# Kernel optimization log

Measured on AMD Instinct MI355X. Metric: run time of the kernel, lower is better.

Reference implementation:

```python
import jax, jax.numpy as jnp
import numpy as np

N = 100000
E = 1600000
D_IN = 128
HEADS = 4
C = 16  # hidden // heads
NEG_SLOPE = 0.2


def setup_inputs() -> dict:
    key = jax.random.key(0)
    ks = jax.random.split(key, 8)
    x = jax.random.normal(ks[0], (N, D_IN), dtype=jnp.float32)
    edge_index = jax.random.randint(ks[1], (2, E), 0, N, dtype=jnp.int32)
    s = 1.0 / np.sqrt(D_IN)
    W_l = jax.random.normal(ks[2], (D_IN, HEADS * C), dtype=jnp.float32) * s
    b_l = jnp.zeros((HEADS * C,), dtype=jnp.float32)
    W_r = jax.random.normal(ks[3], (D_IN, HEADS * C), dtype=jnp.float32) * s
    b_r = jnp.zeros((HEADS * C,), dtype=jnp.float32)
    att = jax.random.normal(ks[4], (HEADS, C), dtype=jnp.float32) * (1.0 / np.sqrt(C))
    bias = jnp.zeros((HEADS * C,), dtype=jnp.float32)
    W_head = jax.random.normal(ks[5], (HEADS * C, 1), dtype=jnp.float32) * (1.0 / np.sqrt(HEADS * C))
    b_head = jnp.zeros((1,), dtype=jnp.float32)
    return {"x": x, "edge_index": edge_index, "W_l": W_l, "b_l": b_l,
            "W_r": W_r, "b_r": b_r, "att": att, "bias": bias,
            "W_head": W_head, "b_head": b_head}


def reference(x, edge_index, W_l, b_l, W_r, b_r, att, bias, W_head, b_head):
    # GATv2Conv (PyG semantics, add_self_loops=True, concat=True)
    n = x.shape[0]
    # add self loops
    loops = jnp.arange(n, dtype=edge_index.dtype)
    src = jnp.concatenate([edge_index[0], loops])  # source j
    dst = jnp.concatenate([edge_index[1], loops])  # target i
    # per-node linear projections -> [N, H, C]
    x_l = (x @ W_l + b_l).reshape(n, HEADS, C)
    x_r = (x @ W_r + b_r).reshape(n, HEADS, C)
    # per-edge attention logits: att . LeakyReLU(x_l[j] + x_r[i])
    e = x_l[src] + x_r[dst]                               # [E', H, C]
    e = jnp.where(e >= 0, e, NEG_SLOPE * e)
    logits = jnp.einsum('ehc,hc->eh', e, att)             # [E', H]
    # segment softmax over incoming edges of each target node
    seg_max = jax.ops.segment_max(logits, dst, num_segments=n)  # [N, H]
    expw = jnp.exp(logits - seg_max[dst])
    seg_sum = jax.ops.segment_sum(expw, dst, num_segments=n)
    alpha = expw / seg_sum[dst]                           # [E', H]
    # weighted scatter-aggregate of source messages
    msg = alpha[:, :, None] * x_l[src]                    # [E', H, C]
    out = jax.ops.segment_sum(msg, dst, num_segments=n)   # [N, H, C]
    out = out.reshape(n, HEADS * C) + bias
    # ReLU + Linear head
    h = jax.nn.relu(out)
    return (h @ W_head + b_head).squeeze(-1)              # [N]
```

## Files before the change

kernel.cpp:

```cpp
#include <hip/hip_runtime.h>
#include <hip/hip_bf16.h>
#include <hip/hip_fp16.h>

#define HC 64
#define D_IN 128
#define NEG_SLOPE 0.2f
#define BCAP 8192
#define L2E 1.44269504f

using f32x4 = __attribute__((ext_vector_type(4))) float;
using f16x8 = __attribute__((ext_vector_type(8))) _Float16;
using f16x2 = __attribute__((ext_vector_type(2))) _Float16;

__global__ void k_iota(int* __restrict__ p, int n) {
    int i = blockIdx.x * blockDim.x + threadIdx.x;
    if (i < n) p[i] = i * BCAP;
}

__global__ __launch_bounds__(256, 3) void k_proj(
    const float* __restrict__ x,
    const float* __restrict__ Wl, const float* __restrict__ bl,
    const float* __restrict__ Wr, const float* __restrict__ br,
    __half* __restrict__ xlh, float* __restrict__ xr, int N) {
    __shared__ _Float16 sWT[128 * 136];
    __shared__ _Float16 sX[32 * 136];
    const int t = threadIdx.x;
    for (int idx = t; idx < 8192; idx += 256) {
        const int k = idx >> 6;
        const int c = idx & 63;
        sWT[c * 136 + k]        = (_Float16)Wl[idx];
        sWT[(c + 64) * 136 + k] = (_Float16)Wr[idx];
    }
    const int lane = t & 63;
    const int wave = t >> 6;
    const int m = lane & 15;
    const int q = lane >> 4;
    float bfu[2];
#pragma unroll
    for (int cc = 0; cc < 2; ++cc) {
        const int ct = wave * 2 + cc;
        const int ch = (ct & 3) * 16 + m;
        bfu[cc] = (ct < 4) ? bl[ch] : br[ch];
    }
    __syncthreads();

    const int ntrip = N >> 5;
    for (int trip = blockIdx.x; trip < ntrip; trip += gridDim.x) {
        const int i0 = trip << 5;
        for (int c = t; c < 1024; c += 256) {
            const int r = c >> 5, c4 = c & 31;
            float4 v = ((const float4*)(x + (size_t)(i0 + r) * D_IN))[c4];
            _Float16* dp = &sX[r * 136 + c4 * 4];
            dp[0] = (_Float16)v.x; dp[1] = (_Float16)v.y;
            dp[2] = (_Float16)v.z; dp[3] = (_Float16)v.w;
        }
        __syncthreads();
        f16x8 af[2][4];
#pragma unroll
        for (int tt = 0; tt < 2; ++tt)
#pragma unroll
            for (int kk = 0; kk < 4; ++kk)
                af[tt][kk] = *(const f16x8*)&sX[(tt * 16 + m) * 136 + kk * 32 + q * 8];
#pragma unroll
        for (int cc = 0; cc < 2; ++cc) {
            const int ct = wave * 2 + cc;
            const _Float16* bp = &sWT[(ct * 16 + m) * 136 + q * 8];
            f32x4 acc0 = {0.f, 0.f, 0.f, 0.f};
            f32x4 acc1 = {0.f, 0.f, 0.f, 0.f};
#pragma unroll
            for (int kk = 0; kk < 4; ++kk) {
                f16x8 bf = *(const f16x8*)(bp + kk * 32);
                acc0 = __builtin_amdgcn_mfma_f32_16x16x32_f16(af[0][kk], bf, acc0, 0, 0, 0);
                acc1 = __builtin_amdgcn_mfma_f32_16x16x32_f16(af[1][kk], bf, acc1, 0, 0, 0);
            }
            const float bv = bfu[cc];
            if (ct < 4) {
                const int ch = ct * 16 + m;
#pragma unroll
                for (int r = 0; r < 4; ++r) {
                    xlh[(size_t)(i0 + q * 4 + r) * HC + ch]      = __float2half(acc0[r] + bv);
                    xlh[(size_t)(i0 + 16 + q * 4 + r) * HC + ch] = __float2half(acc1[r] + bv);
                }
            } else {
                const int ch = (ct - 4) * 16 + m;
#pragma unroll
                for (int r = 0; r < 4; ++r) {
                    xr[(size_t)(i0 + q * 4 + r) * HC + ch]      = acc0[r] + bv;
                    xr[(size_t)(i0 + 16 + q * 4 + r) * HC + ch] = acc1[r] + bv;
                }
            }
        }
        __syncthreads();
    }
}

__global__ __launch_bounds__(256) void k_scat1(const int* __restrict__ src,
                                               const int* __restrict__ dst, int E,
                                               int* __restrict__ bfill,
                                               unsigned* __restrict__ coarse) {
    __shared__ int h[512], bl[512], cur[512];
    for (int t = threadIdx.x; t < 512; t += 256) { h[t] = 0; cur[t] = 0; }
    __syncthreads();
    const int beg = blockIdx.x * 4096;
    const int end = min(beg + 4096, E);
    for (int p = beg + threadIdx.x; p < end; p += 256)
        atomicAdd(&h[dst[p] >> 8], 1);
    __syncthreads();
    for (int t = threadIdx.x; t < 512; t += 256)
        bl[t] = h[t] ? atomicAdd(&bfill[t], h[t]) : 0;
    __syncthreads();
    for (int p = beg + threadIdx.x; p < end; p += 256) {
        const int d = dst[p];
        const int bin = d >> 8;
        const int r = atomicAdd(&cur[bin], 1);
        coarse[bl[bin] + r] = ((unsigned)src[p] << 8) | (unsigned)(d & 255);
    }
}

__global__ __launch_bounds__(256) void k_sort2(const unsigned* __restrict__ coarse,
                                               const int* __restrict__ bfill,
                                               int* __restrict__ row_off,
                                               int* __restrict__ endo,
                                               int* __restrict__ sorted_src, int N) {
    __shared__ int cnt[256], lds[256];
    const int t = threadIdx.x;
    const int b = blockIdx.x;
    const int eb = b * BCAP;
    const int ee = bfill[b];
    cnt[t] = 0;
    __syncthreads();
    for (int p = eb + t; p < ee; p += 256)
        atomicAdd(&cnt[coarse[p] & 255], 1);
    __syncthreads();
    const int c = cnt[t];
    lds[t] = c;
    __syncthreads();
    for (int o = 1; o < 256; o <<= 1) {
        int v = (t >= o) ? lds[t - o] : 0;
        __syncthreads();
        lds[t] += v;
        __syncthreads();
    }
    const int ex = lds[t] - c;
    const int node = (b << 8) + t;
    if (node < N) {
        row_off[node] = eb + ex;
        endo[node]    = eb + ex + c;
    }
    __syncthreads();
    cnt[t] = ex;
    __syncthreads();
    for (int p = eb + t; p < ee; p += 256) {
        const unsigned e = coarse[p];
        const int r = atomicAdd(&cnt[e & 255], 1);
        sorted_src[eb + r] = (int)(e >> 8);
    }
}

__device__ __forceinline__ float redpair(float v) {
    int a = __builtin_amdgcn_update_dpp(0, __float_as_int(v), 0xB1, 0xF, 0xF, true);
    return v + __int_as_float(a);
}

__global__ __launch_bounds__(256) void k_agg(
    const __half* __restrict__ xlh, const float* __restrict__ xr,
    const float* __restrict__ att, const float* __restrict__ bias,
    const float* __restrict__ Wh, const float* __restrict__ bh,
    const int* __restrict__ row_off, const int* __restrict__ endo,
    const int* __restrict__ sorted_src, float* __restrict__ out, int N) {
    const int wave = threadIdx.x >> 6;
    const int lane = threadIdx.x & 63;
    const int i = blockIdx.x * 4 + wave;
    if (i >= N) return;
    const int sub  = lane & 7;
    const int slot = lane >> 3;

    const _Float16* xlhp = (const _Float16*)xlh;
    const float4 atA = *(const float4*)(att + 8 * sub);
    const float4 atB = *(const float4*)(att + 8 * sub + 4);
    f16x2 at[4];
    at[0][0] = (_Float16)(atA.x * L2E); at[0][1] = (_Float16)(atA.y * L2E);
    at[1][0] = (_Float16)(atA.z * L2E); at[1][1] = (_Float16)(atA.w * L2E);
    at[2][0] = (_Float16)(atB.x * L2E); at[2][1] = (_Float16)(atB.y * L2E);
    at[3][0] = (_Float16)(atB.z * L2E); at[3][1] = (_Float16)(atB.w * L2E);
    const f16x2 c02 = {(_Float16)NEG_SLOPE, (_Float16)NEG_SLOPE};

    const float4 xrA = *(const float4*)(xr + ((size_t)i << 6) + 8 * sub);
    const float4 xrB = *(const float4*)(xr + ((size_t)i << 6) + 8 * sub + 4);
    f16x2 xri[4];
    xri[0][0] = (_Float16)xrA.x; xri[0][1] = (_Float16)xrA.y;
    xri[1][0] = (_Float16)xrA.z; xri[1][1] = (_Float16)xrA.w;
    xri[2][0] = (_Float16)xrB.x; xri[2][1] = (_Float16)xrB.y;
    xri[3][0] = (_Float16)xrB.z; xri[3][1] = (_Float16)xrB.w;

    const uint4 xliraw = *(const uint4*)(xlhp + ((size_t)i << 6) + 8 * sub);
    f16x2 xli[4];
    xli[0] = __builtin_bit_cast(f16x2, xliraw.x);
    xli[1] = __builtin_bit_cast(f16x2, xliraw.y);
    xli[2] = __builtin_bit_cast(f16x2, xliraw.z);
    xli[3] = __builtin_bit_cast(f16x2, xliraw.w);

    float t0 = 0.f;
#pragma unroll
    for (int c = 0; c < 4; ++c) {
        f16x2 w = xli[c] + xri[c];
        w = __builtin_elementwise_max(w, w * c02);
        t0 = __builtin_amdgcn_fdot2(at[c], w, t0, false);
    }
    t0 = redpair(t0);
    const float pe0 = (slot == 0) ? exp2f(t0) : 0.f;
    float s = pe0;
    float a[8];
#pragma unroll
    for (int c = 0; c < 4; ++c) {
        a[2 * c]     = pe0 * (float)xli[c][0];
        a[2 * c + 1] = pe0 * (float)xli[c][1];
    }

    int p = row_off[i];
    const int end = endo[i];

#define EDGE_GROUP(JEXPR, PRED)                                              \
    {                                                                        \
        const int jj = (JEXPR);                                              \
        const uint4 raw = *(const uint4*)(xlhp + ((size_t)jj << 6) + 8 * sub);\
        f16x2 xv[4];                                                         \
        xv[0] = __builtin_bit_cast(f16x2, raw.x);                            \
        xv[1] = __builtin_bit_cast(f16x2, raw.y);                            \
        xv[2] = __builtin_bit_cast(f16x2, raw.z);                            \
        xv[3] = __builtin_bit_cast(f16x2, raw.w);                            \
        float tt = 0.f;                                                      \
        _Pragma("unroll")                                                    \
        for (int c = 0; c < 4; ++c) {                                        \
            f16x2 w = xv[c] + xri[c];                                        \
            w = __builtin_elementwise_max(w, w * c02);                       \
            tt = __builtin_amdgcn_fdot2(at[c], w, tt, false);                \
        }                                                                    \
        tt = redpair(tt);                                                    \
        const float pe = (PRED) ? exp2f(tt) : 0.f;                           \
        s += pe;                                                             \
        _Pragma("unroll")                                                    \
        for (int c = 0; c < 4; ++c) {                                        \
            a[2 * c]     = fmaf(pe, (float)xv[c][0], a[2 * c]);              \
            a[2 * c + 1] = fmaf(pe, (float)xv[c][1], a[2 * c + 1]);          \
        }                                                                    \
    }

    for (; p + 16 <= end; p += 16) {
        const int j0 = sorted_src[p + slot];
        const int j1 = sorted_src[p + 8 + slot];
        EDGE_GROUP(j0, true)
        EDGE_GROUP(j1, true)
    }
    if (p + 8 <= end) {
        const int j0 = sorted_src[p + slot];
        EDGE_GROUP(j0, true)
        p += 8;
    }
    const int rem = end - p;
    if (rem > 0) {
        const int idx = p + slot;
        const int j0 = sorted_src[(idx < end) ? idx : (end - 1)];
        EDGE_GROUP(j0, slot < rem)
    }
#undef EDGE_GROUP

    s += __shfl_xor(s, 8);  s += __shfl_xor(s, 16);  s += __shfl_xor(s, 32);
#pragma unroll
    for (int c = 0; c < 8; ++c) {
        a[c] += __shfl_xor(a[c], 8);
        a[c] += __shfl_xor(a[c], 16);
        a[c] += __shfl_xor(a[c], 32);
    }

    const float4 biA = *(const float4*)(bias + 8 * sub);
    const float4 biB = *(const float4*)(bias + 8 * sub + 4);
    const float4 whA = *(const float4*)(Wh + 8 * sub);
    const float4 whB = *(const float4*)(Wh + 8 * sub + 4);
    const float inv = 1.f / s;
    float y = fmaxf(a[0] * inv + biA.x, 0.f) * whA.x
            + fmaxf(a[1] * inv + biA.y, 0.f) * whA.y
            + fmaxf(a[2] * inv + biA.z, 0.f) * whA.z
            + fmaxf(a[3] * inv + biA.w, 0.f) * whA.w
            + fmaxf(a[4] * inv + biB.x, 0.f) * whB.x
            + fmaxf(a[5] * inv + biB.y, 0.f) * whB.y
            + fmaxf(a[6] * inv + biB.z, 0.f) * whB.z
            + fmaxf(a[7] * inv + biB.w, 0.f) * whB.w;
    y += __shfl_xor(y, 1);
    y += __shfl_xor(y, 2);
    y += __shfl_xor(y, 4);
    if (lane == 0) out[i] = y + bh[0];
}

extern "C" void kernel_launch(void* const* d_in, const int* in_sizes, int n_in,
                              void* d_out, int out_size, void* d_ws, size_t ws_size,
                              hipStream_t stream) {
    const float* x   = (const float*)d_in[0];
    const int*   ei  = (const int*)d_in[1];
    const float* Wl  = (const float*)d_in[2];
    const float* bl  = (const float*)d_in[3];
    const float* Wr  = (const float*)d_in[4];
    const float* br  = (const float*)d_in[5];
    const float* att = (const float*)d_in[6];
    const float* bias= (const float*)d_in[7];
    const float* Wh  = (const float*)d_in[8];
    const float* bh  = (const float*)d_in[9];
    float* out = (float*)d_out;

    const int N = in_sizes[0] / D_IN;
    const int E = in_sizes[1] / 2;
    const int* src = ei;
    const int* dst = ei + E;
    const int nbkt = (N + 255) / 256;

    auto align = [](size_t v) { return (v + 255) & ~(size_t)255; };
    char* ws = (char*)d_ws;
    size_t off = 0;
    __half* xlh     = (__half*)(ws + off);   off = align(off + (size_t)N * HC * 2);
    float* xr       = (float*)(ws + off);    off = align(off + (size_t)N * HC * 4);
    int*   row_off  = (int*)(ws + off);      off = align(off + (size_t)N * 4);
    int*   endo     = (int*)(ws + off);      off = align(off + (size_t)N * 4);
    int*   bfill    = (int*)(ws + off);      off = align(off + 512 * 4);
    int*   sorted   = (int*)(ws + off);      off = align(off + (size_t)nbkt * BCAP * 4);
    unsigned* coarse= (unsigned*)(ws + off); off = align(off + (size_t)nbkt * BCAP * 4);
    (void)ws_size;

    k_iota<<<2, 256, 0, stream>>>(bfill, 512);

    k_proj<<<1024, 256, 0, stream>>>(x, Wl, bl, Wr, br, xlh, xr, N);

    k_scat1<<<(E + 4095) / 4096, 256, 0, stream>>>(src, dst, E, bfill, coarse);
    k_sort2<<<nbkt, 256, 0, stream>>>(coarse, bfill, row_off, endo, sorted, N);

    k_agg<<<(N + 3) / 4, 256, 0, stream>>>(xlh, xr, att, bias, Wh, bh,
                                           row_off, endo, sorted, out, N);
}
```

Before: 226.1 us.

## Fuse per-bucket CSR sort into aggregation kernel with 64-node LDS buckets

Drops the separate second-pass sort kernel. Edges are now bucketed into 64-node bins, and each aggregation block sorts its bin's edges by destination in shared memory before its four waves process 16 nodes each. This removes the global writes and reads of sorted_src, row_off and endo, plus one launch. The scatter pass now reads edges with vectorized int4 loads. In exchange there are far fewer blocks, each wave works through its nodes one after another, bucket capacity is fixed at 1536 edges, and the dynamically indexed edge register array may spill.

```diff
diff --git a/kernel.cpp b/kernel.cpp
--- a/kernel.cpp
+++ b/kernel.cpp
@@ -5,7 +5,9 @@
 #define HC 64
 #define D_IN 128
 #define NEG_SLOPE 0.2f
-#define BCAP 8192
+#define BK 64
+#define BCAP2 1536
+#define NBIN 2048
 #define L2E 1.44269504f
 
 using f32x4 = __attribute__((ext_vector_type(4))) float;
@@ -14,7 +16,7 @@
 
 __global__ void k_iota(int* __restrict__ p, int n) {
     int i = blockIdx.x * blockDim.x + threadIdx.x;
-    if (i < n) p[i] = i * BCAP;
+    if (i < n) p[i] = i * BCAP2;
 }
 
 __global__ __launch_bounds__(256, 3) void k_proj(
@@ -98,62 +100,45 @@
                                                const int* __restrict__ dst, int E,
                                                int* __restrict__ bfill,
                                                unsigned* __restrict__ coarse) {
-    __shared__ int h[512], bl[512], cur[512];
-    for (int t = threadIdx.x; t < 512; t += 256) { h[t] = 0; cur[t] = 0; }
+    __shared__ int h[NBIN], bl[NBIN], cur[NBIN];
+    const int t = threadIdx.x;
+    for (int i = t; i < NBIN; i += 256) { h[i] = 0; cur[i] = 0; }
     __syncthreads();
     const int beg = blockIdx.x * 4096;
-    const int end = min(beg + 4096, E);
-    for (int p = beg + threadIdx.x; p < end; p += 256)
-        atomicAdd(&h[dst[p] >> 8], 1);
-    __syncthreads();
-    for (int t = threadIdx.x; t < 512; t += 256)
-        bl[t] = h[t] ? atomicAdd(&bfill[t], h[t]) : 0;
-    __syncthreads();
-    for (int p = beg + threadIdx.x; p < end; p += 256) {
-        const int d = dst[p];
-        const int bin = d >> 8;
-        const int r = atomicAdd(&cur[bin], 1);
-        coarse[bl[bin] + r] = ((unsigned)src[p] << 8) | (unsigned)(d & 255);
-    }
-}
-
-__global__ __launch_bounds__(256) void k_sort2(const unsigned* __restrict__ coarse,
-                                               const int* __restrict__ bfill,
-                                               int* __restrict__ row_off,
-                                               int* __restrict__ endo,
-                                               int* __restrict__ sorted_src, int N) {
-    __shared__ int cnt[256], lds[256];
-    const int t = threadIdx.x;
-    const int b = blockIdx.x;
-    const int eb = b * BCAP;
-    const int ee = bfill[b];
-    cnt[t] = 0;
-    __syncthreads();
-    for (int p = eb + t; p < ee; p += 256)
-        atomicAdd(&cnt[coarse[p] & 255], 1);
-    __syncthreads();
-    const int c = cnt[t];
-    lds[t] = c;
-    __syncthreads();
-    for (int o = 1; o < 256; o <<= 1) {
-        int v = (t >= o) ? lds[t - o] : 0;
-        __syncthreads();
-        lds[t] += v;
-        __syncthreads();
-    }
-    const int ex = lds[t] - c;
-    const int node = (b << 8) + t;
-    if (node < N) {
-        row_off[node] = eb + ex;
-        endo[node]    = eb + ex + c;
-    }
-    __syncthreads();
-    cnt[t] = ex;
-    __syncthreads();
-    for (int p = eb + t; p < ee; p += 256) {
-        const unsigned e = coarse[p];
-        const int r = atomicAdd(&cnt[e & 255], 1);
-        sorted_src[eb + r] = (int)(e >> 8);
+    int4 d4[4], s4[4];
+#pragma unroll
+    for (int r = 0; r < 4; ++r) {
+        const int idx = beg + 4 * t + r * 1024;
+        if (idx < E) {
+            d4[r] = *(const int4*)(dst + idx);
+            s4[r] = *(const int4*)(src + idx);
+        } else { d4[r] = make_int4(-1, -1, -1, -1); }
+    }
+#pragma unroll
+    for (int r = 0; r < 4; ++r) {
+        if (d4[r].x >= 0) {
+            atomicAdd(&h[d4[r].x >> 6], 1);
+            atomicAdd(&h[d4[r].y >> 6], 1);
+            atomicAdd(&h[d4[r].z >> 6], 1);
+            atomicAdd(&h[d4[r].w >> 6], 1);
+        }
+    }
+    __syncthreads();
+    for (int i = t; i < NBIN; i += 256)
+        bl[i] = h[i] ? atomicAdd(&bfill[i], h[i]) : 0;
+    __syncthreads();
+#pragma unroll
+    for (int r = 0; r < 4; ++r) {
+        if (d4[r].x >= 0) {
+            const int dd[4] = {d4[r].x, d4[r].y, d4[r].z, d4[r].w};
+            const int ss[4] = {s4[r].x, s4[r].y, s4[r].z, s4[r].w};
+#pragma unroll
+            for (int j = 0; j < 4; ++j) {
+                const int bin = dd[j] >> 6;
+                const int pos = atomicAdd(&cur[bin], 1);
+                coarse[bl[bin] + pos] = ((unsigned)ss[j] << 6) | (unsigned)(dd[j] & 63);
+            }
+        }
     }
 }
 
@@ -162,20 +147,51 @@
     return v + __int_as_float(a);
 }
 
-__global__ __launch_bounds__(256) void k_agg(
+__global__ __launch_bounds__(256) void k_aggs(
     const __half* __restrict__ xlh, const float* __restrict__ xr,
     const float* __restrict__ att, const float* __restrict__ bias,
     const float* __restrict__ Wh, const float* __restrict__ bh,
-    const int* __restrict__ row_off, const int* __restrict__ endo,
-    const int* __restrict__ sorted_src, float* __restrict__ out, int N) {
-    const int wave = threadIdx.x >> 6;
-    const int lane = threadIdx.x & 63;
-    const int i = blockIdx.x * 4 + wave;
-    if (i >= N) return;
+    const int* __restrict__ bfill, const unsigned* __restrict__ coarse,
+    float* __restrict__ out, int N) {
+    __shared__ int s_src[BCAP2];
+    __shared__ int s_cnt[BK], s_off[BK], s_cur[BK], s_scan[BK];
+    const int t = threadIdx.x;
+    const int b = blockIdx.x;
+    const int eb = b * BCAP2;
+    const int ee = bfill[b];
+    if (t < BK) { s_cnt[t] = 0; s_cur[t] = 0; }
+    __syncthreads();
+    unsigned er[6]; int nr = 0;
+#pragma unroll
+    for (int r = 0; r < 6; ++r) {
+        const int idx = eb + t + r * 256;
+        if (idx < ee) er[nr++] = coarse[idx];
+    }
+    for (int k = 0; k < nr; ++k) atomicAdd(&s_cnt[er[k] & 63], 1);
+    __syncthreads();
+    if (t < BK) s_scan[t] = s_cnt[t];
+    __syncthreads();
+    for (int o = 1; o < BK; o <<= 1) {
+        int v = (t < BK && t >= o) ? s_scan[t - o] : 0;
+        __syncthreads();
+        if (t < BK) s_scan[t] += v;
+        __syncthreads();
+    }
+    if (t < BK) s_off[t] = s_scan[t] - s_cnt[t];
+    __syncthreads();
+    for (int k = 0; k < nr; ++k) {
+        const int bin = er[k] & 63;
+        const int pos = atomicAdd(&s_cur[bin], 1);
+        s_src[s_off[bin] + pos] = (int)(er[k] >> 6);
+    }
+    __syncthreads();
+
+    const int wave = t >> 6;
+    const int lane = t & 63;
     const int sub  = lane & 7;
     const int slot = lane >> 3;
-
     const _Float16* xlhp = (const _Float16*)xlh;
+
     const float4 atA = *(const float4*)(att + 8 * sub);
     const float4 atB = *(const float4*)(att + 8 * sub + 4);
     f16x2 at[4];
@@ -184,42 +200,51 @@
     at[2][0] = (_Float16)(atB.x * L2E); at[2][1] = (_Float16)(atB.y * L2E);
     at[3][0] = (_Float16)(atB.z * L2E); at[3][1] = (_Float16)(atB.w * L2E);
     const f16x2 c02 = {(_Float16)NEG_SLOPE, (_Float16)NEG_SLOPE};
-
-    const float4 xrA = *(const float4*)(xr + ((size_t)i << 6) + 8 * sub);
-    const float4 xrB = *(const float4*)(xr + ((size_t)i << 6) + 8 * sub + 4);
-    f16x2 xri[4];
-    xri[0][0] = (_Float16)xrA.x; xri[0][1] = (_Float16)xrA.y;
-    xri[1][0] = (_Float16)xrA.z; xri[1][1] = (_Float16)xrA.w;
-    xri[2][0] = (_Float16)xrB.x; xri[2][1] = (_Float16)xrB.y;
-    xri[3][0] = (_Float16)xrB.z; xri[3][1] = (_Float16)xrB.w;
-
-    const uint4 xliraw = *(const uint4*)(xlhp + ((size_t)i << 6) + 8 * sub);
-    f16x2 xli[4];
-    xli[0] = __builtin_bit_cast(f16x2, xliraw.x);
-    xli[1] = __builtin_bit_cast(f16x2, xliraw.y);
-    xli[2] = __builtin_bit_cast(f16x2, xliraw.z);
-    xli[3] = __builtin_bit_cast(f16x2, xliraw.w);
-
-    float t0 = 0.f;
-#pragma unroll
-    for (int c = 0; c < 4; ++c) {
-        f16x2 w = xli[c] + xri[c];
-        w = __builtin_elementwise_max(w, w * c02);
-        t0 = __builtin_amdgcn_fdot2(at[c], w, t0, false);
-    }
-    t0 = redpair(t0);
-    const float pe0 = (slot == 0) ? exp2f(t0) : 0.f;
-    float s = pe0;
-    float a[8];
-#pragma unroll
-    for (int c = 0; c < 4; ++c) {
-        a[2 * c]     = pe0 * (float)xli[c][0];
-        a[2 * c + 1] = pe0 * (float)xli[c][1];
-    }
-
-    int p = row_off[i];
-    const int end = endo[i];
-
+    const float4 biA = *(const float4*)(bias + 8 * sub);
+    const float4 biB = *(const float4*)(bias + 8 * sub + 4);
+    const float4 whA = *(const float4*)(Wh + 8 * sub);
+    const float4 whB = *(const float4*)(Wh + 8 * sub + 4);
+    const float bhv = bh[0];
+
+    for (int k16 = 0; k16 < 16; ++k16) {
+        const int nl = wave + 4 * k16;
+        const int i = (b << 6) + nl;
+        if (i >= N) continue;
+        const int beg = s_off[nl];
+        const int cnt = s_cnt[nl];
+
+        const float4 xrA = *(const float4*)(xr + ((size_t)i << 6) + 8 * sub);
+        const float4 xrB = *(const float4*)(xr + ((size_t)i << 6) + 8 * sub + 4);
+        f16x2 xri[4];
+        xri[0][0] = (_Float16)xrA.x; xri[0][1] = (_Float16)xrA.y;
+        xri[1][0] = (_Float16)xrA.z; xri[1][1] = (_Float16)xrA.w;
+        xri[2][0] = (_Float16)xrB.x; xri[2][1] = (_Float16)xrB.y;
+        xri[3][0] = (_Float16)xrB.z; xri[3][1] = (_Float16)xrB.w;
+        const uint4 xliraw = *(const uint4*)(xlhp + ((size_t)i << 6) + 8 * sub);
+        f16x2 xli[4];
+        xli[0] = __builtin_bit_cast(f16x2, xliraw.x);
+        xli[1] = __builtin_bit_cast(f16x2, xliraw.y);
+        xli[2] = __builtin_bit_cast(f16x2, xliraw.z);
+        xli[3] = __builtin_bit_cast(f16x2, xliraw.w);
+
+        float t0 = 0.f;
+#pragma unroll
+        for (int c = 0; c < 4; ++c) {
+            f16x2 w = xli[c] + xri[c];
+            w = __builtin_elementwise_max(w, w * c02);
+            t0 = __builtin_amdgcn_fdot2(at[c], w, t0, false);
+        }
+        t0 = redpair(t0);
+        const float pe0 = (slot == 0) ? exp2f(t0) : 0.f;
+        float s = pe0;
+        float a[8];
+#pragma unroll
+        for (int c = 0; c < 4; ++c) {
+            a[2 * c]     = pe0 * (float)xli[c][0];
+            a[2 * c + 1] = pe0 * (float)xli[c][1];
+        }
+
+        int p = 0;
 #define EDGE_GROUP(JEXPR, PRED)                                              \
     {                                                                        \
         const int jj = (JEXPR);                                              \
@@ -245,51 +270,46 @@
             a[2 * c + 1] = fmaf(pe, (float)xv[c][1], a[2 * c + 1]);          \
         }                                                                    \
     }
-
-    for (; p + 16 <= end; p += 16) {
-        const int j0 = sorted_src[p + slot];
-        const int j1 = sorted_src[p + 8 + slot];
-        EDGE_GROUP(j0, true)
-        EDGE_GROUP(j1, true)
-    }
-    if (p + 8 <= end) {
-        const int j0 = sorted_src[p + slot];
-        EDGE_GROUP(j0, true)
-        p += 8;
-    }
-    const int rem = end - p;
-    if (rem > 0) {
-        const int idx = p + slot;
-        const int j0 = sorted_src[(idx < end) ? idx : (end - 1)];
-        EDGE_GROUP(j0, slot < rem)
-    }
+        for (; p + 16 <= cnt; p += 16) {
+            const int j0 = s_src[beg + p + slot];
+            const int j1 = s_src[beg + p + 8 + slot];
+            EDGE_GROUP(j0, true)
+            EDGE_GROUP(j1, true)
+        }
+        if (p + 8 <= cnt) {
+            const int j0 = s_src[beg + p + slot];
+            EDGE_GROUP(j0, true)
+            p += 8;
+        }
+        const int rem = cnt - p;
+        if (rem > 0) {
+            const int idx = p + slot;
+            const int j0 = s_src[beg + ((idx < cnt) ? idx : (cnt - 1))];
+            EDGE_GROUP(j0, slot < rem)
+        }
 #undef EDGE_GROUP
 
-    s += __shfl_xor(s, 8);  s += __shfl_xor(s, 16);  s += __shfl_xor(s, 32);
-#pragma unroll
-    for (int c = 0; c < 8; ++c) {
-        a[c] += __shfl_xor(a[c], 8);
-        a[c] += __shfl_xor(a[c], 16);
-        a[c] += __shfl_xor(a[c], 32);
-    }
-
-    const float4 biA = *(const float4*)(bias + 8 * sub);
-    const float4 biB = *(const float4*)(bias + 8 * sub + 4);
-    const float4 whA = *(const float4*)(Wh + 8 * sub);
-    const float4 whB = *(const float4*)(Wh + 8 * sub + 4);
-    const float inv = 1.f / s;
-    float y = fmaxf(a[0] * inv + biA.x, 0.f) * whA.x
-            + fmaxf(a[1] * inv + biA.y, 0.f) * whA.y
-            + fmaxf(a[2] * inv + biA.z, 0.f) * whA.z
-            + fmaxf(a[3] * inv + biA.w, 0.f) * whA.w
-            + fmaxf(a[4] * inv + biB.x, 0.f) * whB.x
-            + fmaxf(a[5] * inv + biB.y, 0.f) * whB.y
-            + fmaxf(a[6] * inv + biB.z, 0.f) * whB.z
-            + fmaxf(a[7] * inv + biB.w, 0.f) * whB.w;
-    y += __shfl_xor(y, 1);
-    y += __shfl_xor(y, 2);
-    y += __shfl_xor(y, 4);
-    if (lane == 0) out[i] = y + bh[0];
+        s += __shfl_xor(s, 8);  s += __shfl_xor(s, 16);  s += __shfl_xor(s, 32);
+#pragma unroll
+        for (int c = 0; c < 8; ++c) {
+            a[c] += __shfl_xor(a[c], 8);
+            a[c] += __shfl_xor(a[c], 16);
+            a[c] += __shfl_xor(a[c], 32);
+        }
+        const float inv = 1.f / s;
+        float y = fmaxf(a[0] * inv + biA.x, 0.f) * whA.x
+                + fmaxf(a[1] * inv + biA.y, 0.f) * whA.y
+                + fmaxf(a[2] * inv + biA.z, 0.f) * whA.z
+                + fmaxf(a[3] * inv + biA.w, 0.f) * whA.w
+                + fmaxf(a[4] * inv + biB.x, 0.f) * whB.x
+                + fmaxf(a[5] * inv + biB.y, 0.f) * whB.y
+                + fmaxf(a[6] * inv + biB.z, 0.f) * whB.z
+                + fmaxf(a[7] * inv + biB.w, 0.f) * whB.w;
+        y += __shfl_xor(y, 1);
+        y += __shfl_xor(y, 2);
+        y += __shfl_xor(y, 4);
+        if (lane == 0) out[i] = y + bhv;
+    }
 }
 
 extern "C" void kernel_launch(void* const* d_in, const int* in_sizes, int n_in,
@@ -311,27 +331,23 @@
     const int E = in_sizes[1] / 2;
     const int* src = ei;
     const int* dst = ei + E;
-    const int nbkt = (N + 255) / 256;
+    const int nbkt = (N + BK - 1) / BK;
 
     auto align = [](size_t v) { return (v + 255) & ~(size_t)255; };
     char* ws = (char*)d_ws;
     size_t off = 0;
     __half* xlh     = (__half*)(ws + off);   off = align(off + (size_t)N * HC * 2);
     float* xr       = (float*)(ws + off);    off = align(off + (size_t)N * HC * 4);
-    int*   row_off  = (int*)(ws + off);      off = align(off + (size_t)N * 4);
-    int*   endo     = (int*)(ws + off);      off = align(off + (size_t)N * 4);
-    int*   bfill    = (int*)(ws + off);      off = align(off + 512 * 4);
-    int*   sorted   = (int*)(ws + off);      off = align(off + (size_t)nbkt * BCAP * 4);
-    unsigned* coarse= (unsigned*)(ws + off); off = align(off + (size_t)nbkt * BCAP * 4);
+    int*   bfill    = (int*)(ws + off);      off = align(off + NBIN * 4);
+    unsigned* coarse= (unsigned*)(ws + off); off = align(off + (size_t)NBIN * BCAP2 * 4);
     (void)ws_size;
 
-    k_iota<<<2, 256, 0, stream>>>(bfill, 512);
+    k_iota<<<8, 256, 0, stream>>>(bfill, NBIN);
 
     k_proj<<<1024, 256, 0, stream>>>(x, Wl, bl, Wr, br, xlh, xr, N);
 
     k_scat1<<<(E + 4095) / 4096, 256, 0, stream>>>(src, dst, E, bfill, coarse);
-    k_sort2<<<nbkt, 256, 0, stream>>>(coarse, bfill, row_off, endo, sorted, N);
-
-    k_agg<<<(N + 3) / 4, 256, 0, stream>>>(xlh, xr, att, bias, Wh, bh,
-                                           row_off, endo, sorted, out, N);
-}
+
+    k_aggs<<<nbkt, 256, 0, stream>>>(xlh, xr, att, bias, Wh, bh,
+                                     bfill, coarse, out, N);
+}
```

Measured after the change: 215.9 us. 1.05x faster.
